# Optimization experiments

Measured on AMD Instinct MI355X. Metric: run time of the kernel, lower is better.

The kernel has to match this reference:

```python
import jax, jax.numpy as jnp
import numpy as np

DIM = 192
WIN = (8, 8)
NUM_HEADS = 6
HEAD_DIM = DIM // NUM_HEADS
SCALE = HEAD_DIM ** -0.5
N = WIN[0] * WIN[1]
NUM_REL = (2 * WIN[0] - 1) * (2 * WIN[1] - 1)


def make_rel_pos_index():
    h = np.arange(WIN[0]); w = np.arange(WIN[1])
    idx = np.stack(np.meshgrid(w, h, indexing='ij')).reshape(2, -1)  # (2, N)
    rel = idx[:, :, None] - idx[:, None, :]                          # (2, N, N)
    rel = np.transpose(rel, (1, 2, 0)).copy()
    rel[:, :, 0] += WIN[0] - 1
    rel[:, :, 1] += WIN[1] - 1
    rel[:, :, 0] *= 2 * WIN[1] - 1
    return np.sum(rel, -1)  # (N, N) int indices into bias table

REL_POS_INDEX = make_rel_pos_index()


def setup_inputs() -> dict:
    key = jax.random.key(0)
    ks = jax.random.split(key, 8)
    B = 2048   # num_windows_per_image (64) * images (32)
    nW = 64
    inputs = jax.random.normal(ks[0], (B, N, DIM), dtype=jnp.float32)
    mask = jax.random.normal(ks[1], (nW, N, N), dtype=jnp.float32)
    w_qkv = jax.random.normal(ks[2], (DIM, 3 * DIM), dtype=jnp.float32) * (DIM ** -0.5)
    b_qkv = jnp.zeros((3 * DIM,), dtype=jnp.float32)
    rpbt = jax.random.normal(ks[3], (NUM_REL, NUM_HEADS), dtype=jnp.float32) * 0.02
    w_proj = jax.random.normal(ks[4], (DIM, DIM), dtype=jnp.float32) * (DIM ** -0.5)
    b_proj = jnp.zeros((DIM,), dtype=jnp.float32)
    return {"inputs": inputs, "mask": mask, "w_qkv": w_qkv, "b_qkv": b_qkv,
            "rpbt": rpbt, "w_proj": w_proj, "b_proj": b_proj}


def reference(inputs, mask, w_qkv, b_qkv, rpbt, w_proj, b_proj):
    batch, n, channels = inputs.shape
    qkv = inputs @ w_qkv + b_qkv                                   # (B, n, 3C)
    qkv = qkv.reshape(batch, n, 3, NUM_HEADS, channels // NUM_HEADS)
    qkv = jnp.transpose(qkv, (2, 0, 3, 1, 4))                      # (3, B, H, n, d)
    q, k, v = qkv[0], qkv[1], qkv[2]
    att = jnp.einsum('bhnd,bhmd->bhnm', q * SCALE, k)              # (B, H, n, n)
    # gather relative position bias: (n, n, H) -> (H, n, n)
    rel_bias = rpbt[REL_POS_INDEX.reshape(-1)].reshape(n, n, NUM_HEADS)
    att = att + jnp.transpose(rel_bias, (2, 0, 1))[None]
    nW = mask.shape[0]
    att = att.reshape(batch // nW, nW, NUM_HEADS, n, n)
    att = att + mask[None, :, None]
    att = att.reshape(-1, NUM_HEADS, n, n)
    att = jax.nn.softmax(att, axis=-1)
    x = jnp.einsum('bhnm,bhmd->bnhd', att, v).reshape(batch, n, channels)
    return x @ w_proj + b_proj
```

## Files before the change

kernel.cpp:

```cpp
#include <hip/hip_runtime.h>
#include <hip/hip_bf16.h>
#include <cstdint>


#define NTOK 64
#define NH 6
#define HD 32
#define WDIM 192
#define SCALE 0.17677669529663689f

typedef __bf16 bf16x8 __attribute__((ext_vector_type(8)));
typedef float f32x4 __attribute__((ext_vector_type(4)));

__device__ inline unsigned short f2bf(float f) {
    union { __bf16 b; unsigned short s; } u;
    u.b = (__bf16)f;
    return u.s;
}

__global__ __launch_bounds__(256) void prep_kernel(
    const float* __restrict__ w_qkv, const float* __restrict__ w_proj,
    const float* __restrict__ rpbt, const float* __restrict__ mask,
    unsigned short* __restrict__ wqkv_f, unsigned short* __restrict__ wproj_f,
    float* __restrict__ comb) {
    int idx = blockIdx.x * 256 + threadIdx.x;
    if (idx < 576 * 192) {
        int j = idx & 7, lane = (idx >> 3) & 63, t = idx >> 9;
        int ks = t % 6, ntile = t / 6;
        int n = ntile * 16 + (lane & 15);
        int k = ks * 32 + (lane >> 4) * 8 + j;
        wqkv_f[idx] = f2bf(w_qkv[k * 576 + n]);
        return;
    }
    int i2 = idx - 576 * 192;
    if (i2 < 192 * 192) {
        int j = i2 & 7, lane = (i2 >> 3) & 63, t = i2 >> 9;
        int ks = t % 6, ntile = t / 6;
        int n = ntile * 16 + (lane & 15);
        int k = ks * 32 + (lane >> 4) * 8 + j;
        wproj_f[i2] = f2bf(w_proj[k * 192 + n]);
        return;
    }
    int i3 = i2 - 192 * 192;
    if (i3 < 64 * NH * NTOK * NTOK) {
        int c = i3 & 63, r = (i3 >> 6) & 63;
        int h = (i3 >> 12) % NH;
        int w = i3 / (NH * 4096);
        int rr = (r >> 3) - (c >> 3) + 7;
        int cc = (r & 7) - (c & 7) + 7;
        comb[i3] = rpbt[(rr * 15 + cc) * NH + h] + mask[w * 4096 + r * 64 + c];
    }
}

__global__ __launch_bounds__(512, 2) void fused_kernel(
    const float* __restrict__ X, const unsigned short* __restrict__ Wqf,
    const float* __restrict__ b_qkv, const unsigned short* __restrict__ Wpf,
    const float* __restrict__ b_proj, const float* __restrict__ comb,
    float* __restrict__ out) {
    __shared__ unsigned short sm[28672];
    unsigned short* lx   = sm;
    unsigned short* lq2  = sm;
    unsigned short* lk2  = sm + 5120;
    unsigned short* lvt2 = sm + 10240;
    unsigned short* lxa  = sm + 14848;

    const int tid = threadIdx.x;
    const int bwin = blockIdx.x;
    const int wave = tid >> 6, lane = tid & 63;
    const int l15 = lane & 15, quad = lane >> 4;
    const int wm = wave >> 2, wn = wave & 3;

    const float4* xg = (const float4*)(X + (size_t)bwin * 64 * 192);
    for (int i = 0; i < 6; i++) {
        int e4 = tid + i * 512;
        int row = e4 / 48, c4 = e4 % 48;
        float4 v = xg[e4];
        union { unsigned short s[4]; uint2 u; } pk;
        pk.s[0] = f2bf(v.x); pk.s[1] = f2bf(v.y);
        pk.s[2] = f2bf(v.z); pk.s[3] = f2bf(v.w);
        *(uint2*)&lx[row * 200 + c4 * 4] = pk.u;
    }
    __syncthreads();

    bf16x8 af[2][6];
    for (int mt = 0; mt < 2; mt++)
        for (int ks = 0; ks < 6; ks++)
            af[mt][ks] = *(const bf16x8*)&lx[(wm * 32 + mt * 16 + l15) * 200 + ks * 32 + quad * 8];
    unsigned short* lspw = sm + 19456 + wave * 1152;

    f32x4 pacc[2][3];
    for (int mt = 0; mt < 2; mt++)
        for (int nt = 0; nt < 3; nt++)
            pacc[mt][nt] = (f32x4){0.f, 0.f, 0.f, 0.f};

    const float* combg = comb + ((size_t)(bwin & 63) * NH) * 4096;

    for (int p = 0; p < 3; p++) {
        const int hl = wm;
        const int mbase = wn * 16;
        const int hg = p * 2 + hl;

        float cmb[4][4];
        #pragma unroll
        for (int j = 0; j < 4; j++)
            #pragma unroll
            for (int r = 0; r < 4; r++)
                cmb[j][r] = combg[hg * 4096 + (mbase + quad * 4 + r) * 64 + j * 16 + l15];

        const unsigned short* wptr[3];
        #pragma unroll
        for (int i = 0; i < 3; i++) {
            int f = wn * 3 + i, c = f >> 2, j = f & 3;
            wptr[i] = Wqf + ((size_t)((c * 12 + p * 4 + j) * 6)) * 512 + lane * 8;
        }
        f32x4 acc[2][3];
        #pragma unroll
        for (int mt = 0; mt < 2; mt++)
            #pragma unroll
            for (int i = 0; i < 3; i++)
                acc[mt][i] = (f32x4){0.f, 0.f, 0.f, 0.f};

        bf16x8 bcur[3], bnxt[3];
        #pragma unroll
        for (int i = 0; i < 3; i++)
            bcur[i] = *(const bf16x8*)(wptr[i]);
        #pragma unroll
        for (int ks = 0; ks < 6; ks++) {
            if (ks < 5) {
                #pragma unroll
                for (int i = 0; i < 3; i++)
                    bnxt[i] = *(const bf16x8*)(wptr[i] + (ks + 1) * 512);
            }
            #pragma unroll
            for (int mt = 0; mt < 2; mt++)
                #pragma unroll
                for (int i = 0; i < 3; i++)
                    acc[mt][i] = __builtin_amdgcn_mfma_f32_16x16x32_bf16(
                        af[mt][ks], bcur[i], acc[mt][i], 0, 0, 0);
            #pragma unroll
            for (int i = 0; i < 3; i++)
                bcur[i] = bnxt[i];
        }
        __syncthreads();
        #pragma unroll
        for (int i = 0; i < 3; i++) {
            int f = wn * 3 + i, c = f >> 2, j = f & 3;
            int cw = j * 16 + l15;
            float bias = b_qkv[c * 192 + p * 64 + cw];
            int hle = cw >> 5, d = cw & 31;
            if (c < 2) {
                unsigned short* dst = (c == 0) ? lq2 : lk2;
                #pragma unroll
                for (int mt = 0; mt < 2; mt++)
                    #pragma unroll
                    for (int r = 0; r < 4; r++) {
                        int t = wm * 32 + mt * 16 + quad * 4 + r;
                        dst[(hle * 64 + t) * 40 + d] = f2bf(acc[mt][i][r] + bias);
                    }
            } else {
                #pragma unroll
                for (int mt = 0; mt < 2; mt++) {
                    union { unsigned short s[4]; uint2 u; } pk;
                    #pragma unroll
                    for (int r = 0; r < 4; r++)
                        pk.s[r] = f2bf(acc[mt][i][r] + bias);
                    int t0 = wm * 32 + mt * 16 + quad * 4;
                    *(uint2*)&lvt2[(hle * 32 + d) * 72 + t0] = pk.u;
                }
            }
        }
        __syncthreads();

        bf16x8 aq = *(const bf16x8*)&lq2[(hl * 64 + mbase + l15) * 40 + quad * 8];
        f32x4 sacc[4];
        #pragma unroll
        for (int j = 0; j < 4; j++) {
            bf16x8 bk = *(const bf16x8*)&lk2[(hl * 64 + j * 16 + l15) * 40 + quad * 8];
            f32x4 z = (f32x4){0.f, 0.f, 0.f, 0.f};
            sacc[j] = __builtin_amdgcn_mfma_f32_16x16x32_bf16(aq, bk, z, 0, 0, 0);
        }

        float pr[4][4], rsum[4];
        #pragma unroll
        for (int r = 0; r < 4; r++) {
            float s0 = sacc[0][r] * SCALE + cmb[0][r];
            float s1 = sacc[1][r] * SCALE + cmb[1][r];
            float s2 = sacc[2][r] * SCALE + cmb[2][r];
            float s3 = sacc[3][r] * SCALE + cmb[3][r];
            float m = fmaxf(fmaxf(s0, s1), fmaxf(s2, s3));
            for (int o = 1; o < 16; o <<= 1) m = fmaxf(m, __shfl_xor(m, o, 64));
            pr[0][r] = __expf(s0 - m); pr[1][r] = __expf(s1 - m);
            pr[2][r] = __expf(s2 - m); pr[3][r] = __expf(s3 - m);
            float su = pr[0][r] + pr[1][r] + pr[2][r] + pr[3][r];
            for (int o = 1; o < 16; o <<= 1) su += __shfl_xor(su, o, 64);
            rsum[r] = su;
        }

        #pragma unroll
        for (int j = 0; j < 4; j++)
            #pragma unroll
            for (int r = 0; r < 4; r++)
                lspw[(quad * 4 + r) * 72 + j * 16 + l15] = f2bf(pr[j][r]);

        f32x4 oacc[2];
        oacc[0] = (f32x4){0.f, 0.f, 0.f, 0.f};
        oacc[1] = (f32x4){0.f, 0.f, 0.f, 0.f};
        #pragma unroll
        for (int kstep = 0; kstep < 2; kstep++) {
            bf16x8 ap = *(const bf16x8*)&lspw[l15 * 72 + kstep * 32 + quad * 8];
            #pragma unroll
            for (int n2 = 0; n2 < 2; n2++) {
                bf16x8 bv = *(const bf16x8*)&lvt2[
                    (hl * 32 + n2 * 16 + l15) * 72 + kstep * 32 + quad * 8];
                oacc[n2] = __builtin_amdgcn_mfma_f32_16x16x32_bf16(ap, bv, oacc[n2], 0, 0, 0);
            }
        }

        bf16x8 pb0[3];
        #pragma unroll
        for (int nt = 0; nt < 3; nt++)
            pb0[nt] = *(const bf16x8*)&Wpf[
                ((size_t)((wn * 3 + nt) * 6 + (p * 2 + 0))) * 512 + lane * 8];

        #pragma unroll
        for (int r = 0; r < 4; r++) {
            float inv = 1.0f / rsum[r];
            int t = mbase + quad * 4 + r;
            #pragma unroll
            for (int n2 = 0; n2 < 2; n2++)
                lxa[t * 72 + hl * 32 + n2 * 16 + l15] = f2bf(oacc[n2][r] * inv);
        }
        __syncthreads();

        bf16x8 pb1[3];
        #pragma unroll
        for (int nt = 0; nt < 3; nt++)
            pb1[nt] = *(const bf16x8*)&Wpf[
                ((size_t)((wn * 3 + nt) * 6 + (p * 2 + 1))) * 512 + lane * 8];
        bf16x8 pf[2][2];
        #pragma unroll
        for (int mt = 0; mt < 2; mt++)
            #pragma unroll
            for (int kk = 0; kk < 2; kk++)
                pf[mt][kk] = *(const bf16x8*)&lxa[
                    (wm * 32 + mt * 16 + l15) * 72 + kk * 32 + quad * 8];
        #pragma unroll
        for (int mt = 0; mt < 2; mt++)
            #pragma unroll
            for (int nt = 0; nt < 3; nt++)
                pacc[mt][nt] = __builtin_amdgcn_mfma_f32_16x16x32_bf16(
                    pf[mt][0], pb0[nt], pacc[mt][nt], 0, 0, 0);
        #pragma unroll
        for (int mt = 0; mt < 2; mt++)
            #pragma unroll
            for (int nt = 0; nt < 3; nt++)
                pacc[mt][nt] = __builtin_amdgcn_mfma_f32_16x16x32_bf16(
                    pf[mt][1], pb1[nt], pacc[mt][nt], 0, 0, 0);
    }

    for (int nt = 0; nt < 3; nt++) {
        int cw = wn * 48 + nt * 16 + l15;
        float bias = b_proj[cw];
        for (int mt = 0; mt < 2; mt++)
            for (int r = 0; r < 4; r++) {
                int t = wm * 32 + mt * 16 + quad * 4 + r;
                out[((size_t)bwin * 64 + t) * 192 + cw] = pacc[mt][nt][r] + bias;
            }
    }
}

extern "C" void kernel_launch(void* const* d_in, const int* in_sizes, int n_in,
                              void* d_out, int out_size, void* d_ws, size_t ws_size,
                              hipStream_t stream) {
    const float* x      = (const float*)d_in[0];
    const float* mask   = (const float*)d_in[1];
    const float* w_qkv  = (const float*)d_in[2];
    const float* b_qkv  = (const float*)d_in[3];
    const float* rpbt   = (const float*)d_in[4];
    const float* w_proj = (const float*)d_in[5];
    const float* b_proj = (const float*)d_in[6];
    float* out = (float*)d_out;

    const int B = in_sizes[0] / (NTOK * WDIM);

    char* ws = (char*)d_ws;
    size_t o = 0;
    unsigned short* Wq = (unsigned short*)(ws + o); o += 576 * 192 * 2;
    unsigned short* Wp = (unsigned short*)(ws + o); o += 192 * 192 * 2;
    float* comb        = (float*)(ws + o);         o += (size_t)64 * NH * NTOK * NTOK * 4;

    const int prep_elems = 576 * 192 + 192 * 192 + 64 * NH * NTOK * NTOK;
    prep_kernel<<<(prep_elems + 255) / 256, 256, 0, stream>>>(
        w_qkv, w_proj, rpbt, mask, Wq, Wp, comb);
    fused_kernel<<<B, 512, 0, stream>>>(
        x, Wq, b_qkv, Wp, b_proj, comb, out);
}
```

Measured before the change: 291.4 us.

## Store bias+mask table in bf16 with vectorized per-lane layout, raise occupancy bound

Precomputes the combined relative-position bias and mask in bf16 instead of fp32, laid out so each lane loads its four row values with one 8-byte load. It also raises the launch-bounds minimum blocks per CU and writes softmax probabilities to LDS inside the row loop to shorten register lifetimes. This is meant to halve bias-table traffic and cut load instruction count. It trades some precision in the additive mask, and the tighter register budget risks spills.

```diff
diff --git a/kernel.cpp b/kernel.cpp
--- a/kernel.cpp
+++ b/kernel.cpp
@@ -18,11 +18,16 @@
     return u.s;
 }
 
+__device__ inline float bfbits2f(unsigned short s) {
+    union { unsigned u; float f; } v; v.u = ((unsigned)s) << 16;
+    return v.f;
+}
+
 __global__ __launch_bounds__(256) void prep_kernel(
     const float* __restrict__ w_qkv, const float* __restrict__ w_proj,
     const float* __restrict__ rpbt, const float* __restrict__ mask,
     unsigned short* __restrict__ wqkv_f, unsigned short* __restrict__ wproj_f,
-    float* __restrict__ comb) {
+    unsigned short* __restrict__ comb_bf) {
     int idx = blockIdx.x * 256 + threadIdx.x;
     if (idx < 576 * 192) {
         int j = idx & 7, lane = (idx >> 3) & 63, t = idx >> 9;
@@ -43,19 +48,23 @@
     }
     int i3 = i2 - 192 * 192;
     if (i3 < 64 * NH * NTOK * NTOK) {
-        int c = i3 & 63, r = (i3 >> 6) & 63;
+        int rr = i3 & 3;
+        int c = (i3 >> 2) & 63;
+        int rb = (i3 >> 8) & 15;
         int h = (i3 >> 12) % NH;
         int w = i3 / (NH * 4096);
-        int rr = (r >> 3) - (c >> 3) + 7;
-        int cc = (r & 7) - (c & 7) + 7;
-        comb[i3] = rpbt[(rr * 15 + cc) * NH + h] + mask[w * 4096 + r * 64 + c];
-    }
-}
-
-__global__ __launch_bounds__(512, 2) void fused_kernel(
+        int r = rb * 4 + rr;
+        int rrd = (r >> 3) - (c >> 3) + 7;
+        int ccd = (r & 7) - (c & 7) + 7;
+        comb_bf[i3] = f2bf(rpbt[(rrd * 15 + ccd) * NH + h]
+                           + mask[w * 4096 + r * 64 + c]);
+    }
+}
+
+__global__ __launch_bounds__(512, 4) void fused_kernel(
     const float* __restrict__ X, const unsigned short* __restrict__ Wqf,
     const float* __restrict__ b_qkv, const unsigned short* __restrict__ Wpf,
-    const float* __restrict__ b_proj, const float* __restrict__ comb,
+    const float* __restrict__ b_proj, const unsigned short* __restrict__ comb_bf,
     float* __restrict__ out) {
     __shared__ unsigned short sm[28672];
     unsigned short* lx   = sm;
@@ -93,19 +102,18 @@
         for (int nt = 0; nt < 3; nt++)
             pacc[mt][nt] = (f32x4){0.f, 0.f, 0.f, 0.f};
 
-    const float* combg = comb + ((size_t)(bwin & 63) * NH) * 4096;
+    const unsigned short* combg = comb_bf + ((size_t)(bwin & 63) * NH) * 4096;
 
     for (int p = 0; p < 3; p++) {
         const int hl = wm;
         const int mbase = wn * 16;
         const int hg = p * 2 + hl;
 
-        float cmb[4][4];
+        uint2 cmbp[4];
         #pragma unroll
         for (int j = 0; j < 4; j++)
-            #pragma unroll
-            for (int r = 0; r < 4; r++)
-                cmb[j][r] = combg[hg * 4096 + (mbase + quad * 4 + r) * 64 + j * 16 + l15];
+            cmbp[j] = *(const uint2*)&combg[
+                (((size_t)hg * 16 + (mbase >> 2) + quad) * 64 + j * 16 + l15) * 4];
 
         const unsigned short* wptr[3];
         #pragma unroll
@@ -180,27 +188,26 @@
             sacc[j] = __builtin_amdgcn_mfma_f32_16x16x32_bf16(aq, bk, z, 0, 0, 0);
         }
 
-        float pr[4][4], rsum[4];
+        float rsum[4];
         #pragma unroll
         for (int r = 0; r < 4; r++) {
-            float s0 = sacc[0][r] * SCALE + cmb[0][r];
-            float s1 = sacc[1][r] * SCALE + cmb[1][r];
-            float s2 = sacc[2][r] * SCALE + cmb[2][r];
-            float s3 = sacc[3][r] * SCALE + cmb[3][r];
+            float s0 = sacc[0][r] * SCALE + bfbits2f(((const unsigned short*)&cmbp[0])[r]);
+            float s1 = sacc[1][r] * SCALE + bfbits2f(((const unsigned short*)&cmbp[1])[r]);
+            float s2 = sacc[2][r] * SCALE + bfbits2f(((const unsigned short*)&cmbp[2])[r]);
+            float s3 = sacc[3][r] * SCALE + bfbits2f(((const unsigned short*)&cmbp[3])[r]);
             float m = fmaxf(fmaxf(s0, s1), fmaxf(s2, s3));
             for (int o = 1; o < 16; o <<= 1) m = fmaxf(m, __shfl_xor(m, o, 64));
-            pr[0][r] = __expf(s0 - m); pr[1][r] = __expf(s1 - m);
-            pr[2][r] = __expf(s2 - m); pr[3][r] = __expf(s3 - m);
-            float su = pr[0][r] + pr[1][r] + pr[2][r] + pr[3][r];
+            float p0 = __expf(s0 - m), p1 = __expf(s1 - m);
+            float p2 = __expf(s2 - m), p3 = __expf(s3 - m);
+            float su = p0 + p1 + p2 + p3;
             for (int o = 1; o < 16; o <<= 1) su += __shfl_xor(su, o, 64);
             rsum[r] = su;
-        }
-
-        #pragma unroll
-        for (int j = 0; j < 4; j++)
-            #pragma unroll
-            for (int r = 0; r < 4; r++)
-                lspw[(quad * 4 + r) * 72 + j * 16 + l15] = f2bf(pr[j][r]);
+            int row = quad * 4 + r;
+            lspw[row * 72 +  0 + l15] = f2bf(p0);
+            lspw[row * 72 + 16 + l15] = f2bf(p1);
+            lspw[row * 72 + 32 + l15] = f2bf(p2);
+            lspw[row * 72 + 48 + l15] = f2bf(p3);
+        }
 
         f32x4 oacc[2];
         oacc[0] = (f32x4){0.f, 0.f, 0.f, 0.f};
@@ -287,11 +294,12 @@
     size_t o = 0;
     unsigned short* Wq = (unsigned short*)(ws + o); o += 576 * 192 * 2;
     unsigned short* Wp = (unsigned short*)(ws + o); o += 192 * 192 * 2;
-    float* comb        = (float*)(ws + o);         o += (size_t)64 * NH * NTOK * NTOK * 4;
+    unsigned short* comb_bf = (unsigned short*)(ws + o);
+    o += (size_t)64 * NH * NTOK * NTOK * 2;
 
     const int prep_elems = 576 * 192 + 192 * 192 + 64 * NH * NTOK * NTOK;
     prep_kernel<<<(prep_elems + 255) / 256, 256, 0, stream>>>(
-        w_qkv, w_proj, rpbt, mask, Wq, Wp, comb);
+        w_qkv, w_proj, rpbt, mask, Wq, Wp, comb_bf);
     fused_kernel<<<B, 512, 0, stream>>>(
-        x, Wq, b_qkv, Wp, b_proj, comb, out);
-}
+        x, Wq, b_qkv, Wp, b_proj, comb_bf, out);
+}
```

Result: slower. 334.6 us (+14.8%).
